# Performance work log

Measured on AMD Instinct MI355X. Metric: run time of the kernel, lower is better.

The kernel has to match this reference:

```python
import jax, jax.numpy as jnp
import numpy as np
from jax import lax

N, D, K, R, T = 200000, 128, 64, 4, 50000
L = 2 * R  # positive + negative relation layers
ITERATIONS = 2


def _l2norm(x, eps=1e-12):
    # torch F.normalize(p=2): x / max(||x||, eps)
    n = jnp.sqrt(jnp.sum(x * x, axis=-1, keepdims=True))
    return x / jnp.maximum(n, eps)


def setup_inputs() -> dict:
    key = jax.random.key(0)
    ks = jax.random.split(key, 8)
    # Unique write targets (a permutation) so the last-write scatter is deterministic;
    # matches input_specs' randint intent (indices uniform in [0, N)).
    perm = jax.random.permutation(ks[0], N)
    subj_idx = perm[:T].astype(jnp.int32)
    obj_idx = perm[T:2 * T].astype(jnp.int32)
    layer_idx = jax.random.randint(ks[1], (T,), 0, L, dtype=jnp.int32)
    memberships = jax.random.randint(ks[2], (N, K), 0, 2, dtype=jnp.int32)
    embedding_m = jax.random.normal(ks[3], (N, D), dtype=jnp.float32)
    # ClassUpdate params: [d+K] -> d
    Wc = jax.random.normal(ks[4], (D + K, D), dtype=jnp.float32) / np.sqrt(D + K)
    bc = jnp.zeros((D,), dtype=jnp.float32)
    # RelationUpdate params, one layer per (relation, polarity): [2d] -> [2d]
    Wr = jax.random.normal(ks[5], (L, 2 * D, 2 * D), dtype=jnp.float32) / np.sqrt(2 * D)
    br = jnp.zeros((L, 2 * D), dtype=jnp.float32)
    return {
        'embedding_m': embedding_m,
        'memberships': memberships,
        'subj_idx': subj_idx,
        'obj_idx': obj_idx,
        'layer_idx': layer_idx,
        'Wc': Wc, 'bc': bc, 'Wr': Wr, 'br': br,
    }


def reference(embedding_m, memberships, subj_idx, obj_idx, layer_idx, Wc, bc, Wr, br):
    mem = memberships.astype(embedding_m.dtype)  # [N, K]
    t_ar = jnp.arange(T)

    def iteration(e, _):
        # --- ClassUpdate: e' = l2norm(tanh([e; m] Wc + bc)) ---
        x = jnp.concatenate([e, mem], axis=1)           # [N, d+K]
        e = _l2norm(jnp.tanh(x @ Wc + bc))              # [N, d]
        # --- RelationUpdates: reads come from the post-class-update snapshot `e`
        pair = jnp.concatenate([e[subj_idx], e[obj_idx]], axis=1)   # [T, 2d]
        # compute through all L relation layers, then select each triple's layer
        out_all = jnp.einsum('tc,lcd->tld', pair, Wr) + br          # [T, L, 2d]
        out = jnp.tanh(out_all[t_ar, layer_idx])                    # [T, 2d]
        new_s = _l2norm(out[:, :D])
        new_o = _l2norm(out[:, D:])
        e_next = e.at[subj_idx].set(new_s).at[obj_idx].set(new_o)
        return e_next, None

    e_final, _ = lax.scan(iteration, embedding_m, None, length=ITERATIONS)
    return e_final
```

## Files before the change

kernel.cpp:

```cpp
#include <hip/hip_runtime.h>
#include <hip/hip_bf16.h>


#define NROWS 200000
#define DD    128
#define KK    64
#define TT    50000
#define LL    8
#define BT    64
#define PADT  50560
#define NPASS 3125

#define NB    100
#define CHB   500
#define PL    8
#define PREPB 268
#define MBB   6250

#define WS_OFFS   0
#define WS_CNT    64
#define WS_BASE   4096
#define WS_BINS   8192
#define WS_WCP    210432
#define WS_WRP    (WS_WCP + 6*8*64*16)
#define WS_MB     (WS_WRP + 8*8*16*64*16)
#define WS_E16    (WS_MB + NROWS*8)
#define WS_NEED   (WS_E16 + (size_t)NROWS*DD*2)

typedef unsigned short u16;
typedef unsigned int   u32;
typedef unsigned long long u64;
typedef unsigned char  u8;
typedef __attribute__((ext_vector_type(8))) short bf16x8;
typedef __attribute__((ext_vector_type(4))) float f32x4;

#define SWZ(row, byte) ((byte) ^ (((row)&7)<<4))

__device__ __forceinline__ u32 bfbits(float f){
  __hip_bfloat16 h = __float2bfloat16(f);
  return (u32)*reinterpret_cast<unsigned short*>(&h);
}
__device__ __forceinline__ u32 pk(float lo, float hi){
  return bfbits(lo) | (bfbits(hi) << 16);
}
__device__ __forceinline__ float qreduce16(float ss){
  ss += __shfl_xor(ss, 1, 64);
  ss += __shfl_xor(ss, 2, 64);
  ss += __shfl_xor(ss, 4, 64);
  ss += __shfl_xor(ss, 8, 64);
  return ss;
}
__device__ __forceinline__ float fast_tanh(float x){
  float a = fabsf(x);
  float e = __expf(-2.0f*a);
  float t = (1.0f - e) * __builtin_amdgcn_rcpf(1.0f + e);
  return copysignf(t, x);
}
__device__ __forceinline__ float rnorm_scale(float ss){
  return __builtin_amdgcn_rcpf(fmaxf(__builtin_amdgcn_sqrtf(ss), 1e-12f));
}
__device__ __forceinline__ void nt_store_u16(u16* p, u16 v){
  __builtin_nontemporal_store(v, p);
}
__device__ __forceinline__ void nt_store_f32(float* p, float v){
  __builtin_nontemporal_store(v, p);
}

__global__ __launch_bounds__(256) void k_prep(
    const float* __restrict__ Wc, const float* __restrict__ Wr,
    uint4* __restrict__ wcp, uint4* __restrict__ wrp,
    const int* __restrict__ layer, int* __restrict__ cnt,
    const int* __restrict__ mem, u8* __restrict__ mb8)
{
  if (blockIdx.x >= PREPB + NB){
    int gid = (blockIdx.x - PREPB - NB)*256 + threadIdx.x;
    const int4* s4 = (const int4*)(mem + (size_t)gid*8);
    int4 a = s4[0], b = s4[1];
    u8 byte = (u8)((a.x!=0) | ((a.y!=0)<<1) | ((a.z!=0)<<2) | ((a.w!=0)<<3)
             | ((b.x!=0)<<4) | ((b.y!=0)<<5) | ((b.z!=0)<<6) | ((b.w!=0)<<7));
    __builtin_nontemporal_store(byte, &mb8[gid]);
    return;
  }
  if (blockIdx.x >= PREPB){
    const int bb = blockIdx.x - PREPB, lane = threadIdx.x;
    if (lane >= 64) return;
    const int lim = bb*CHB + CHB;
    int i0 = bb*CHB + lane*PL, i1 = i0 + PL; if (i1 > lim) i1 = lim;
    int c[LL] = {0,0,0,0,0,0,0,0};
    for (int i = i0; i < i1; ++i){
      int l = layer[i];
      #pragma unroll
      for (int k = 0; k < LL; ++k) c[k] += (l == k);
    }
    #pragma unroll
    for (int k = 0; k < LL; ++k){
      int v = c[k];
      v += __shfl_xor(v, 1, 64); v += __shfl_xor(v, 2, 64);
      v += __shfl_xor(v, 4, 64); v += __shfl_xor(v, 8, 64);
      v += __shfl_xor(v, 16, 64); v += __shfl_xor(v, 32, 64);
      if (lane == k) cnt[bb*LL + k] = v;
    }
    return;
  }
  int id = blockIdx.x*blockDim.x + threadIdx.x;
  if (id < 3072){
    int lane = id & 63, nt = (id >> 6) & 7, kt = id >> 9;
    int k0 = kt*32 + (lane>>4)*8, n = nt*16 + (lane&15);
    u32 p[4];
    #pragma unroll
    for (int e2 = 0; e2 < 4; ++e2)
      p[e2] = pk(Wc[(k0 + 2*e2)*DD + n], Wc[(k0 + 2*e2 + 1)*DD + n]);
    wcp[id] = make_uint4(p[0], p[1], p[2], p[3]);
  } else if (id < 3072 + 65536){
    int id2 = id - 3072;
    int lane = id2 & 63, nt = (id2>>6) & 15, kt = (id2>>10) & 7, l = id2 >> 13;
    int k0 = kt*32 + (lane>>4)*8, n = nt*16 + (lane&15);
    const float* w = Wr + (size_t)l*65536;
    u32 p[4];
    #pragma unroll
    for (int e2 = 0; e2 < 4; ++e2)
      p[e2] = pk(w[(k0 + 2*e2)*256 + n], w[(k0 + 2*e2 + 1)*256 + n]);
    wrp[id2] = make_uint4(p[0], p[1], p[2], p[3]);
  }
}

__global__ __launch_bounds__(64) void k_bin2(const int* __restrict__ cnt,
                                             int* __restrict__ offs,
                                             int* __restrict__ gbase,
                                             int* __restrict__ bins)
{
  __shared__ int pre[NB][LL];
  __shared__ int tot[LL], soffs[LL+1];
  const int t = threadIdx.x;
  if (t < LL){
    int acc = 0;
    for (int bb = 0; bb < NB; ++bb){ pre[bb][t] = acc; acc += cnt[bb*LL + t]; }
    tot[t] = acc;
  }
  __syncthreads();
  if (t == 0){
    int acc = 0;
    for (int l = 0; l < LL; ++l){
      soffs[l] = acc; offs[l] = acc;
      acc += ((tot[l] + BT - 1)/BT)*BT;
    }
    soffs[LL] = acc; offs[LL] = acc;
  }
  __syncthreads();
  for (int idx = t; idx < NB*LL; idx += 64){
    int bb = idx >> 3, k = idx & 7;
    gbase[idx] = soffs[k] + pre[bb][k];
  }
  const int k = t >> 3, sub = t & 7;
  const int sz = soffs[k+1] - soffs[k];
  for (int i = tot[k] + sub; i < sz; i += 8) bins[soffs[k] + i] = -1;
}

__global__ __launch_bounds__(64) void k_bin3(const int* __restrict__ layer,
                                             const int* __restrict__ gbase,
                                             int* __restrict__ bins)
{
  const int bb = blockIdx.x, lane = threadIdx.x;
  const int lim = bb*CHB + CHB;
  int i0 = bb*CHB + lane*PL, i1 = i0 + PL; if (i1 > lim) i1 = lim;
  int c[LL] = {0,0,0,0,0,0,0,0};
  for (int i = i0; i < i1; ++i){
    int l = layer[i];
    #pragma unroll
    for (int k = 0; k < LL; ++k) c[k] += (l == k);
  }
  int start[LL];
  #pragma unroll
  for (int k = 0; k < LL; ++k){
    int v = c[k];
    #pragma unroll
    for (int d = 1; d < 64; d <<= 1){
      int u = __shfl_up(v, d, 64);
      if (lane >= d) v += u;
    }
    start[k] = gbase[bb*LL + k] + v - c[k];
  }
  for (int i = i0; i < i1; ++i){
    int l = layer[i];
    #pragma unroll
    for (int k = 0; k < LL; ++k)
      if (l == k) bins[start[k]++] = i;
  }
}

template<bool S16, bool W16, bool WF32>
__global__ __launch_bounds__(256) void k_class(
    const float* __restrict__ srcf, const u16* __restrict__ src16,
    u16* __restrict__ e16, float* __restrict__ dstf,
    const u64* __restrict__ mbits,
    const uint4* __restrict__ wcp, const float* __restrict__ bc)
{
  __shared__ u16   sA[64*192];
  __shared__ float sPart[64][4];

  const int tid = threadIdx.x;
  const int lane = tid & 63, wid = tid >> 6;
  const int colj = lane & 15, qw = lane >> 4;
  const int rowbase = blockIdx.x * 64;

  int erow[4], ecol[4];
  uint4  eA[4];
  float4 fA[4][2];
  #pragma unroll
  for (int v = 0; v < 4; ++v){
    int f = (v*256 + tid) * 8;
    erow[v] = f >> 7; ecol[v] = f & 127;
    if constexpr (S16){
      eA[v] = *(const uint4*)(src16 + (size_t)(rowbase+erow[v])*DD + ecol[v]);
    } else {
      const float4* s4 = (const float4*)(srcf + (size_t)(rowbase+erow[v])*DD + ecol[v]);
      fA[v][0] = s4[0]; fA[v][1] = s4[1];
    }
  }
  const u64 mv = mbits[rowbase + (tid >> 2)];

  bf16x8 wf[6][2];
  #pragma unroll
  for (int kt = 0; kt < 6; ++kt)
    #pragma unroll
    for (int j = 0; j < 2; ++j)
      wf[kt][j] = *(const bf16x8*)&wcp[(kt*8 + 2*wid + j)*64 + lane];
  const float b0 = bc[(2*wid)*16 + colj];
  const float b1 = bc[(2*wid+1)*16 + colj];

  #pragma unroll
  for (int v = 0; v < 4; ++v){
    uint4 out;
    if constexpr (S16){
      out = eA[v];
    } else {
      float4 a = fA[v][0], b = fA[v][1];
      out = make_uint4(pk(a.x,a.y), pk(a.z,a.w), pk(b.x,b.y), pk(b.z,b.w));
    }
    *(uint4*)((char*)sA + erow[v]*384 + SWZ(erow[v], ecol[v]*2)) = out;
  }
  {
    const int r = tid >> 2, q = tid & 3;
    u32 s = (u32)(mv >> (q*16)) & 0xFFFFu;
    u32 p[8];
    #pragma unroll
    for (int jj = 0; jj < 8; ++jj){
      u32 lo = (s >> (2*jj))     & 1u;
      u32 hi = (s >> (2*jj + 1)) & 1u;
      p[jj] = (lo ? 0x3F80u : 0u) | (hi ? 0x3F800000u : 0u);
    }
    *(uint4*)((char*)sA + r*384 + SWZ(r, 256 + q*32))      = make_uint4(p[0],p[1],p[2],p[3]);
    *(uint4*)((char*)sA + r*384 + SWZ(r, 256 + q*32 + 16)) = make_uint4(p[4],p[5],p[6],p[7]);
  }
  __syncthreads();

  f32x4 acc[4][2];
  #pragma unroll
  for (int m = 0; m < 4; ++m){
    acc[m][0] = (f32x4){0.f,0.f,0.f,0.f};
    acc[m][1] = (f32x4){0.f,0.f,0.f,0.f};
  }
  #pragma unroll
  for (int m = 0; m < 4; ++m){
    int row = m*16 + colj;
    #pragma unroll
    for (int kt = 0; kt < 6; ++kt){
      bf16x8 afr = *(bf16x8*)((char*)sA + row*384 + SWZ(row, kt*64 + qw*16));
      acc[m][0] = __builtin_amdgcn_mfma_f32_16x16x32_bf16(afr, wf[kt][0], acc[m][0], 0,0,0);
      acc[m][1] = __builtin_amdgcn_mfma_f32_16x16x32_bf16(afr, wf[kt][1], acc[m][1], 0,0,0);
    }
  }
  #pragma unroll
  for (int m = 0; m < 4; ++m){
    #pragma unroll
    for (int r = 0; r < 4; ++r){
      float t0 = fast_tanh(acc[m][0][r] + b0);
      float t1 = fast_tanh(acc[m][1][r] + b1);
      acc[m][0][r] = t0; acc[m][1][r] = t1;
      float ss = qreduce16(t0*t0 + t1*t1);
      if (colj == 0) sPart[m*16 + qw*4 + r][wid] = ss;
    }
  }
  __syncthreads();
  #pragma unroll
  for (int m = 0; m < 4; ++m){
    #pragma unroll
    for (int r = 0; r < 4; ++r){
      int tri = m*16 + qw*4 + r;
      f32x4 p = *(f32x4*)sPart[tri];
      float sc = rnorm_scale(p[0] + p[1] + p[2] + p[3]);
      int grow = rowbase + tri;
      float v0 = acc[m][0][r]*sc, v1 = acc[m][1][r]*sc;
      int c0 = (2*wid)*16 + colj;
      if constexpr (W16){
        nt_store_u16(&e16[(size_t)grow*DD + c0],      (u16)bfbits(v0));
        nt_store_u16(&e16[(size_t)grow*DD + c0 + 16], (u16)bfbits(v1));
      }
      if constexpr (WF32){
        nt_store_f32(&dstf[(size_t)grow*DD + c0],      v0);
        nt_store_f32(&dstf[(size_t)grow*DD + c0 + 16], v1);
      }
    }
  }
}

template<bool S16, bool W16, bool WF32>
__global__ __launch_bounds__(256) void k_rel(
    const float* __restrict__ ef32, u16* __restrict__ e16,
    float* __restrict__ dstf,
    const int* __restrict__ subj, const int* __restrict__ obj,
    const uint4* __restrict__ wrp, const float* __restrict__ br,
    const int* __restrict__ offs, const int* __restrict__ bins)
{
  __shared__ u16   sA[64*256];
  __shared__ float sBr[256];
  __shared__ float sPart[BT][4];
  __shared__ int   sS[BT], sO[BT];

  const int tid  = threadIdx.x;
  const int base = blockIdx.x * BT;
  if (base >= offs[LL]) return;
  int l = 0;
  while (l < LL-1 && base >= offs[l+1]) ++l;

  const int lane = tid & 63, wid = tid >> 6;
  const int colj = lane & 15, qw = lane >> 4;

  const uint4* wb = wrp + (size_t)l*8192 + lane;
  bf16x8 wf[8][4];
  #pragma unroll
  for (int n = 0; n < 4; ++n){
    wf[0][n] = *(const bf16x8*)&wb[(0*16 + wid*4 + n)*64];
    wf[1][n] = *(const bf16x8*)&wb[(1*16 + wid*4 + n)*64];
  }

  sBr[tid] = br[l*256 + tid];

  const int ti = tid >> 2, q = tid & 3;
  int id = bins[base + ti];
  int rs = -1, ro = -1;
  if (id >= 0){ rs = subj[id]; ro = obj[id]; }
  if (q == 0){ sS[ti] = rs; sO[ti] = ro; }
  const int rr = (q < 2) ? rs : ro;
  if constexpr (S16){
    const u16* srcp = e16 + (size_t)rr*DD + (q & 1)*64;
    #pragma unroll
    for (int j = 0; j < 8; ++j){
      uint4 w = (id >= 0) ? ((const uint4*)srcp)[j] : make_uint4(0u,0u,0u,0u);
      *(uint4*)((char*)sA + ti*512 + SWZ(ti, q*128 + j*16)) = w;
    }
  } else {
    const float* srcp = ef32 + (size_t)rr*DD + (q & 1)*64;
    #pragma unroll
    for (int j = 0; j < 8; ++j){
      uint4 w;
      if (id >= 0){
        float4 a = ((const float4*)srcp)[2*j], b = ((const float4*)srcp)[2*j+1];
        w = make_uint4(pk(a.x,a.y), pk(a.z,a.w), pk(b.x,b.y), pk(b.z,b.w));
      } else w = make_uint4(0u,0u,0u,0u);
      *(uint4*)((char*)sA + ti*512 + SWZ(ti, q*128 + j*16)) = w;
    }
  }
  __syncthreads();

  f32x4 acc[4][4];
  #pragma unroll
  for (int m = 0; m < 4; ++m)
    #pragma unroll
    for (int n = 0; n < 4; ++n) acc[m][n] = (f32x4){0.f,0.f,0.f,0.f};

  #pragma unroll
  for (int kt = 0; kt < 8; ++kt){
    if (kt + 2 < 8){
      #pragma unroll
      for (int n = 0; n < 4; ++n)
        wf[kt+2][n] = *(const bf16x8*)&wb[((kt+2)*16 + wid*4 + n)*64];
    }
    #pragma unroll
    for (int m = 0; m < 4; ++m){
      int row = m*16 + colj;
      bf16x8 afr = *(bf16x8*)((char*)sA + row*512 + SWZ(row, kt*64 + qw*16));
      #pragma unroll
      for (int n = 0; n < 4; ++n)
        acc[m][n] = __builtin_amdgcn_mfma_f32_16x16x32_bf16(afr, wf[kt][n], acc[m][n], 0,0,0);
    }
  }

  #pragma unroll
  for (int m = 0; m < 4; ++m){
    #pragma unroll
    for (int n = 0; n < 4; ++n){
      float b = sBr[(wid*4 + n)*16 + colj];
      #pragma unroll
      for (int r = 0; r < 4; ++r)
        acc[m][n][r] = fast_tanh(acc[m][n][r] + b);
    }
    #pragma unroll
    for (int r = 0; r < 4; ++r){
      float ss = acc[m][0][r]*acc[m][0][r] + acc[m][1][r]*acc[m][1][r]
               + acc[m][2][r]*acc[m][2][r] + acc[m][3][r]*acc[m][3][r];
      ss = qreduce16(ss);
      if (colj == 0) sPart[m*16 + qw*4 + r][wid] = ss;
    }
  }
  __syncthreads();

  const int h = wid >> 1;
  #pragma unroll
  for (int m = 0; m < 4; ++m){
    #pragma unroll
    for (int r = 0; r < 4; ++r){
      int tri = m*16 + qw*4 + r;
      int row = h ? sO[tri] : sS[tri];
      if (row < 0) continue;
      float ss = sPart[tri][2*h] + sPart[tri][2*h + 1];
      float sc = rnorm_scale(ss);
      #pragma unroll
      for (int n = 0; n < 4; ++n){
        int cc = (wid*4 + n)*16 + colj - h*DD;
        float v = acc[m][n][r]*sc;
        if constexpr (W16)
          nt_store_u16(&e16[(size_t)row*DD + cc], (u16)bfbits(v));
        if constexpr (WF32)
          nt_store_f32(&dstf[(size_t)row*DD + cc], v);
      }
    }
  }
}

extern "C" void kernel_launch(void* const* d_in, const int* in_sizes, int n_in,
                              void* d_out, int out_size, void* d_ws, size_t ws_size,
                              hipStream_t stream) {
  (void)in_sizes; (void)n_in; (void)out_size;
  const float* emb  = (const float*)d_in[0];
  const int*   mem  = (const int*)  d_in[1];
  const int*   subj = (const int*)  d_in[2];
  const int*   obj  = (const int*)  d_in[3];
  const int*   lay  = (const int*)  d_in[4];
  const float* Wc   = (const float*)d_in[5];
  const float* bc   = (const float*)d_in[6];
  const float* Wr   = (const float*)d_in[7];
  const float* br   = (const float*)d_in[8];

  float* e   = (float*)d_out;
  char*  wsb = (char*)d_ws;
  int*   offs  = (int*)(wsb + WS_OFFS);
  int*   cnt   = (int*)(wsb + WS_CNT);
  int*   gbase = (int*)(wsb + WS_BASE);
  int*   bins  = (int*)(wsb + WS_BINS);
  uint4* wcp   = (uint4*)(wsb + WS_WCP);
  uint4* wrp   = (uint4*)(wsb + WS_WRP);
  u64*   mbits = (u64*)(wsb + WS_MB);
  u8*    mb8   = (u8*)(wsb + WS_MB);
  u16*   e16   = (u16*)(wsb + WS_E16);

  k_prep<<<PREPB + NB + MBB, 256, 0, stream>>>(Wc, Wr, wcp, wrp, lay, cnt, mem, mb8);
  k_bin2<<<1, 64, 0, stream>>>(cnt, offs, gbase, bins);
  k_bin3<<<NB, 64, 0, stream>>>(lay, gbase, bins);

  if (ws_size >= WS_NEED){
    k_class<false,true,false><<<NPASS, 256, 0, stream>>>(
        emb, nullptr, e16, nullptr, mbits, wcp, bc);
    k_rel<true,true,false><<<PADT/BT, 256, 0, stream>>>(
        nullptr, e16, nullptr, subj, obj, wrp, br, offs, bins);
    k_class<true,false,true><<<NPASS, 256, 0, stream>>>(
        nullptr, e16, nullptr, e, mbits, wcp, bc);
    k_rel<false,false,true><<<PADT/BT, 256, 0, stream>>>(
        e, nullptr, e, subj, obj, wrp, br, offs, bins);
  } else {
    k_class<false,false,true><<<NPASS, 256, 0, stream>>>(
        emb, nullptr, nullptr, e, mbits, wcp, bc);
    k_rel<false,false,true><<<PADT/BT, 256, 0, stream>>>(
        e, nullptr, e, subj, obj, wrp, br, offs, bins);
    k_class<true,false,true><<<NPASS, 256, 0, stream>>>(
        nullptr, nullptr, nullptr, e, mbits, wcp, bc);
    k_rel<false,false,true><<<PADT/BT, 256, 0, stream>>>(
        e, nullptr, e, subj, obj, wrp, br, offs, bins);
  }
}
```

Measured before the change: 172.2 us.

## Load class-update A fragments directly from global, drop LDS staging and syncs

Result: slower. 206.9 us (+20.2%).

```diff
diff --git a/kernel.cpp b/kernel.cpp
--- a/kernel.cpp
+++ b/kernel.cpp
@@ -64,6 +64,14 @@
 }
 __device__ __forceinline__ void nt_store_f32(float* p, float v){
   __builtin_nontemporal_store(v, p);
+}
+__device__ __forceinline__ bf16x8 mem_frag(u32 byte){
+  union { uint4 q; bf16x8 f; } u;
+  u.q.x = ((byte&1u)  ?0x3F80u:0u) | ((byte&2u)  ?0x3F800000u:0u);
+  u.q.y = ((byte&4u)  ?0x3F80u:0u) | ((byte&8u)  ?0x3F800000u:0u);
+  u.q.z = ((byte&16u) ?0x3F80u:0u) | ((byte&32u) ?0x3F800000u:0u);
+  u.q.w = ((byte&64u) ?0x3F80u:0u) | ((byte&128u)?0x3F800000u:0u);
+  return u.f;
 }
 
 __global__ __launch_bounds__(256) void k_prep(
@@ -195,111 +203,73 @@
     const u64* __restrict__ mbits,
     const uint4* __restrict__ wcp, const float* __restrict__ bc)
 {
-  __shared__ u16   sA[64*192];
-  __shared__ float sPart[64][4];
-
   const int tid = threadIdx.x;
   const int lane = tid & 63, wid = tid >> 6;
   const int colj = lane & 15, qw = lane >> 4;
   const int rowbase = blockIdx.x * 64;
-
-  int erow[4], ecol[4];
-  uint4  eA[4];
-  float4 fA[4][2];
-  #pragma unroll
-  for (int v = 0; v < 4; ++v){
-    int f = (v*256 + tid) * 8;
-    erow[v] = f >> 7; ecol[v] = f & 127;
-    if constexpr (S16){
-      eA[v] = *(const uint4*)(src16 + (size_t)(rowbase+erow[v])*DD + ecol[v]);
-    } else {
-      const float4* s4 = (const float4*)(srcf + (size_t)(rowbase+erow[v])*DD + ecol[v]);
-      fA[v][0] = s4[0]; fA[v][1] = s4[1];
-    }
-  }
-  const u64 mv = mbits[rowbase + (tid >> 2)];
-
-  bf16x8 wf[6][2];
-  #pragma unroll
-  for (int kt = 0; kt < 6; ++kt)
-    #pragma unroll
-    for (int j = 0; j < 2; ++j)
-      wf[kt][j] = *(const bf16x8*)&wcp[(kt*8 + 2*wid + j)*64 + lane];
-  const float b0 = bc[(2*wid)*16 + colj];
-  const float b1 = bc[(2*wid+1)*16 + colj];
-
-  #pragma unroll
-  for (int v = 0; v < 4; ++v){
-    uint4 out;
-    if constexpr (S16){
-      out = eA[v];
-    } else {
-      float4 a = fA[v][0], b = fA[v][1];
-      out = make_uint4(pk(a.x,a.y), pk(a.z,a.w), pk(b.x,b.y), pk(b.z,b.w));
-    }
-    *(uint4*)((char*)sA + erow[v]*384 + SWZ(erow[v], ecol[v]*2)) = out;
-  }
-  {
-    const int r = tid >> 2, q = tid & 3;
-    u32 s = (u32)(mv >> (q*16)) & 0xFFFFu;
-    u32 p[8];
-    #pragma unroll
-    for (int jj = 0; jj < 8; ++jj){
-      u32 lo = (s >> (2*jj))     & 1u;
-      u32 hi = (s >> (2*jj + 1)) & 1u;
-      p[jj] = (lo ? 0x3F80u : 0u) | (hi ? 0x3F800000u : 0u);
-    }
-    *(uint4*)((char*)sA + r*384 + SWZ(r, 256 + q*32))      = make_uint4(p[0],p[1],p[2],p[3]);
-    *(uint4*)((char*)sA + r*384 + SWZ(r, 256 + q*32 + 16)) = make_uint4(p[4],p[5],p[6],p[7]);
-  }
-  __syncthreads();
-
-  f32x4 acc[4][2];
-  #pragma unroll
-  for (int m = 0; m < 4; ++m){
-    acc[m][0] = (f32x4){0.f,0.f,0.f,0.f};
-    acc[m][1] = (f32x4){0.f,0.f,0.f,0.f};
-  }
-  #pragma unroll
-  for (int m = 0; m < 4; ++m){
-    int row = m*16 + colj;
+  const int arow = rowbase + wid*16 + colj;
+
+  bf16x8 afr[6];
+  if constexpr (S16){
+    const u16* rp = src16 + (size_t)arow*DD + qw*8;
+    #pragma unroll
+    for (int kt = 0; kt < 4; ++kt){
+      uint4 q = *(const uint4*)(rp + kt*32);
+      afr[kt] = *(bf16x8*)&q;
+    }
+  } else {
+    const float* rp = srcf + (size_t)arow*DD + qw*8;
+    float4 fq[8];
+    #pragma unroll
+    for (int kt = 0; kt < 4; ++kt){
+      fq[2*kt]   = *(const float4*)(rp + kt*32);
+      fq[2*kt+1] = *(const float4*)(rp + kt*32 + 4);
+    }
+    #pragma unroll
+    for (int kt = 0; kt < 4; ++kt){
+      float4 a = fq[2*kt], b = fq[2*kt+1];
+      uint4 q = make_uint4(pk(a.x,a.y), pk(a.z,a.w), pk(b.x,b.y), pk(b.z,b.w));
+      afr[kt] = *(bf16x8*)&q;
+    }
+  }
+  const u64 mv = mbits[arow];
+  afr[4] = mem_frag((u32)(mv >> (qw*8)) & 0xFFu);
+  afr[5] = mem_frag((u32)(mv >> (32 + qw*8)) & 0xFFu);
+
+  float b[8];
+  #pragma unroll
+  for (int nt = 0; nt < 8; ++nt) b[nt] = bc[nt*16 + colj];
+
+  f32x4 acc[8];
+  #pragma unroll
+  for (int nt = 0; nt < 8; ++nt) acc[nt] = (f32x4){0.f,0.f,0.f,0.f};
+  #pragma unroll
+  for (int nt = 0; nt < 8; ++nt){
     #pragma unroll
     for (int kt = 0; kt < 6; ++kt){
-      bf16x8 afr = *(bf16x8*)((char*)sA + row*384 + SWZ(row, kt*64 + qw*16));
-      acc[m][0] = __builtin_amdgcn_mfma_f32_16x16x32_bf16(afr, wf[kt][0], acc[m][0], 0,0,0);
-      acc[m][1] = __builtin_amdgcn_mfma_f32_16x16x32_bf16(afr, wf[kt][1], acc[m][1], 0,0,0);
-    }
-  }
-  #pragma unroll
-  for (int m = 0; m < 4; ++m){
-    #pragma unroll
-    for (int r = 0; r < 4; ++r){
-      float t0 = fast_tanh(acc[m][0][r] + b0);
-      float t1 = fast_tanh(acc[m][1][r] + b1);
-      acc[m][0][r] = t0; acc[m][1][r] = t1;
-      float ss = qreduce16(t0*t0 + t1*t1);
-      if (colj == 0) sPart[m*16 + qw*4 + r][wid] = ss;
-    }
-  }
-  __syncthreads();
-  #pragma unroll
-  for (int m = 0; m < 4; ++m){
-    #pragma unroll
-    for (int r = 0; r < 4; ++r){
-      int tri = m*16 + qw*4 + r;
-      f32x4 p = *(f32x4*)sPart[tri];
-      float sc = rnorm_scale(p[0] + p[1] + p[2] + p[3]);
-      int grow = rowbase + tri;
-      float v0 = acc[m][0][r]*sc, v1 = acc[m][1][r]*sc;
-      int c0 = (2*wid)*16 + colj;
-      if constexpr (W16){
-        nt_store_u16(&e16[(size_t)grow*DD + c0],      (u16)bfbits(v0));
-        nt_store_u16(&e16[(size_t)grow*DD + c0 + 16], (u16)bfbits(v1));
-      }
-      if constexpr (WF32){
-        nt_store_f32(&dstf[(size_t)grow*DD + c0],      v0);
-        nt_store_f32(&dstf[(size_t)grow*DD + c0 + 16], v1);
-      }
+      bf16x8 w = *(const bf16x8*)&wcp[(kt*8 + nt)*64 + lane];
+      acc[nt] = __builtin_amdgcn_mfma_f32_16x16x32_bf16(afr[kt], w, acc[nt], 0,0,0);
+    }
+  }
+
+  #pragma unroll
+  for (int r = 0; r < 4; ++r){
+    float t[8], ss = 0.f;
+    #pragma unroll
+    for (int nt = 0; nt < 8; ++nt){
+      t[nt] = fast_tanh(acc[nt][r] + b[nt]);
+      ss += t[nt]*t[nt];
+    }
+    ss = qreduce16(ss);
+    float sc = rnorm_scale(ss);
+    const int orow = rowbase + wid*16 + qw*4 + r;
+    #pragma unroll
+    for (int nt = 0; nt < 8; ++nt){
+      float v = t[nt]*sc;
+      if constexpr (W16)
+        nt_store_u16(&e16[(size_t)orow*DD + nt*16 + colj], (u16)bfbits(v));
+      if constexpr (WF32)
+        nt_store_f32(&dstf[(size_t)orow*DD + nt*16 + colj], v);
     }
   }
 }
@@ -472,8 +442,8 @@
         emb, nullptr, nullptr, e, mbits, wcp, bc);
     k_rel<false,false,true><<<PADT/BT, 256, 0, stream>>>(
         e, nullptr, e, subj, obj, wrp, br, offs, bins);
-    k_class<true,false,true><<<NPASS, 256, 0, stream>>>(
-        nullptr, nullptr, nullptr, e, mbits, wcp, bc);
+    k_class<false,false,true><<<NPASS, 256, 0, stream>>>(
+        e, nullptr, nullptr, e, mbits, wcp, bc);
     k_rel<false,false,true><<<PADT/BT, 256, 0, stream>>>(
         e, nullptr, e, subj, obj, wrp, br, offs, bins);
   }
```
